# Kernel tuning notes

Measured on AMD Instinct MI355X. Metric: run time of the kernel, lower is better.

The kernel has to match this reference:

```python
import jax, jax.numpy as jnp
import numpy as np

NINP = 1024
NHID = 1024
STEPS = 8
INITRANGE = 0.04
T, B = 256, 64

# DARTS_V1 recurrent genotype: (activation, predecessor-state index)
GENOTYPE = [("sigmoid", 0), ("relu", 1), ("relu", 1), ("identity", 1),
            ("tanh", 2), ("sigmoid", 5), ("tanh", 3), ("relu", 5)]

ACT = {
    "tanh": jnp.tanh,
    "relu": jax.nn.relu,
    "sigmoid": jax.nn.sigmoid,
    "identity": lambda x: x,
    "selu": jax.nn.selu,
}


def setup_inputs() -> dict:
    key = jax.random.key(0)
    k_in, k_w0, k_ws = jax.random.split(key, 3)
    inputs = jax.random.normal(k_in, (T, B, NINP), dtype=jnp.float32)
    hidden = jnp.zeros((1, B, NHID), dtype=jnp.float32)
    W0 = jax.random.uniform(k_w0, (NINP + NHID, 2 * NHID),
                            minval=-INITRANGE, maxval=INITRANGE, dtype=jnp.float32)
    Ws = jax.random.uniform(k_ws, (STEPS, NHID, 2 * NHID),
                            minval=-INITRANGE, maxval=INITRANGE, dtype=jnp.float32)
    return {"inputs": inputs, "hidden": hidden, "W0": W0, "Ws": Ws}


def _cell(x, h_prev, W0, Ws):
    # init state: highway combine of gated candidate with previous hidden
    xh = jnp.concatenate([x, h_prev], axis=-1)            # [B, ninp+nhid]
    c0, h0 = jnp.split(xh @ W0, 2, axis=-1)               # [B, nhid] each
    s0 = h_prev + jax.nn.sigmoid(c0) * (jnp.tanh(h0) - h_prev)
    states = [s0]
    for i, (name, pred) in enumerate(GENOTYPE):
        s_prev = states[pred]
        c, h = jnp.split(s_prev @ Ws[i], 2, axis=-1)      # [B, nhid] each
        s = s_prev + jax.nn.sigmoid(c) * (ACT[name](h) - s_prev)
        states.append(s)
    # output = mean over the DAG intermediate states (concat = range(1, steps+1))
    return jnp.mean(jnp.stack(states[1:], axis=0), axis=0)


def reference(inputs, hidden, W0, Ws):
    h0 = hidden[0]                                        # [B, nhid]

    def step(h, x_t):
        h_new = _cell(x_t, h, W0, Ws)
        return h_new, h_new

    _, hiddens = jax.lax.scan(step, h0, inputs)           # [T, B, nhid]
    return hiddens
```

## Files before the change

kernel.cpp:

```cpp
#include <hip/hip_runtime.h>
#include <math.h>


typedef __attribute__((ext_vector_type(8))) _Float16 half8;
typedef __attribute__((ext_vector_type(4))) float f32x4;
typedef __attribute__((ext_vector_type(4))) unsigned int u32x4;
typedef __attribute__((ext_vector_type(8))) unsigned short us8;

#define NH 1024
#define SCALE 2048.f
#define INVS  (1.f/2048.f)
#define WF_BYTES 83886080ull
#define FA_BYTES 1572864ull
#define T_STEPS  256

__device__ __forceinline__ float sigf(float x){ return 1.f/(1.f+__expf(-x)); }
__device__ __forceinline__ void limbs2(float x, _Float16& a, _Float16& b){
    a = (_Float16)x; b = (_Float16)((x - (float)a)*SCALE);
}

struct Pre { const float* W0; const float* Ws; unsigned short* wf; };

__global__ __launch_bounds__(256) void preconv(Pre d) {
    int gid  = blockIdx.x * 4 + (threadIdx.x >> 6);
    int lane = threadIdx.x & 63;
    const float* W; unsigned short* dst; int nks, cg, ks;
    if (gid < 8192) {
        W = d.W0; dst = d.wf; nks = 64; cg = gid >> 6; ks = gid & 63;
    } else {
        int g = gid - 8192; int mm = g >> 12; int wi = g & 4095;
        W   = d.Ws + (size_t)mm * (1024 * 2048);
        dst = d.wf + 8388608ull + (size_t)mm * 4194304ull;
        nks = 32; cg = wi >> 5; ks = wi & 31;
    }
    int c  = cg * 16 + (lane & 15);
    int kb = ks * 32 + (lane >> 4) * 8;
    half8 h0, h1;
    #pragma unroll
    for (int j = 0; j < 8; ++j) {
        _Float16 p, q; limbs2(W[(size_t)(kb + j) * 2048 + c], p, q);
        h0[j] = p; h1[j] = q;
    }
    unsigned short* o = dst + ((size_t)cg * nks + ks) * 1024 + lane * 8;
    *(half8*)o         = h0;
    *(half8*)(o + 512) = h1;
}

__global__ __launch_bounds__(256) void initk(const float* hidden, char* fa, unsigned* flags) {
    int gid = blockIdx.x * 256 + threadIdx.x;
    if (gid < 1536) flags[gid] = (gid < 256) ? 1u : 0u;
    #pragma unroll
    for (int e = 0; e < 4; ++e) {
        int i = gid * 4 + e;
        int row = i >> 10, col = i & 1023;
        int rt = row >> 4, rowf = row & 15;
        int ksp = col >> 5, kin = col & 31;
        int lanep = (kin >> 3) * 16 + rowf;
        size_t off = (size_t)rt * 65536 + ((size_t)ksp * 64 + lanep) * 32 + (kin & 7) * 4;
        _Float16 u0, u1; limbs2(hidden[i], u0, u1);
        unsigned pk = (unsigned)__builtin_bit_cast(unsigned short, u0) |
                      ((unsigned)__builtin_bit_cast(unsigned short, u1) << 16);
        *(unsigned*)(fa + off) = pk;
    }
}

__device__ __forceinline__ void aload(const char* fa, int ks, int lane, half8& a0, half8& a1) {
    const char* p = fa + ((size_t)ks * 64 + lane) * 32;
    us8 q0 = *(const us8*)p;
    us8 q1 = *(const us8*)(p + 16);
    a0 = __builtin_bit_cast(half8, __builtin_shufflevector(q0, q1, 0,2,4,6,8,10,12,14));
    a1 = __builtin_bit_cast(half8, __builtin_shufflevector(q0, q1, 1,3,5,7,9,11,13,15));
}
__device__ __forceinline__ half8 ldw(const unsigned short* p) { return *(const half8*)p; }
__device__ __forceinline__ void mfma6(half8 a0, half8 a1, half8 w0, half8 w1,
                                      f32x4& x0, f32x4& x1) {
    x0 = __builtin_amdgcn_mfma_f32_16x16x32_f16(a0, w0, x0, 0, 0, 0);
    x1 = __builtin_amdgcn_mfma_f32_16x16x32_f16(a0, w1, x1, 0, 0, 0);
    x1 = __builtin_amdgcn_mfma_f32_16x16x32_f16(a1, w0, x1, 0, 0, 0);
}
__device__ __forceinline__ void rwrite1(float* arena, int wave, int lane,
        f32x4 c0, f32x4 c1, f32x4 h0, f32x4 h1) {
    float* b = arena + wave * 512;
    #pragma unroll
    for (int r = 0; r < 4; ++r) {
        b[lane * 4 + r]       = c0[r] + c1[r] * INVS;
        b[256 + lane * 4 + r] = h0[r] + h1[r] * INVS;
    }
}
__device__ __forceinline__ void rsum1(const float* arena, int idx, float& cs, float& hs) {
    float c = 0.f, h = 0.f;
    #pragma unroll
    for (int w = 0; w < 8; ++w) {
        c += arena[w * 512 + idx];
        h += arena[w * 512 + 256 + idx];
    }
    cs = c; hs = h;
}
__device__ __forceinline__ void fstore(char* fa, int offp, float v) {
    _Float16 u0, u1; limbs2(v, u0, u1);
    unsigned pk = (unsigned)__builtin_bit_cast(unsigned short, u0) |
                  ((unsigned)__builtin_bit_cast(unsigned short, u1) << 16);
    __hip_atomic_store((unsigned*)(fa + offp), pk, __ATOMIC_RELAXED, __HIP_MEMORY_SCOPE_AGENT);
}
template<int ACQ>
__device__ __forceinline__ void pollw(unsigned* f, unsigned tgt, int lane) {
    unsigned v = __hip_atomic_load(f + lane, __ATOMIC_RELAXED, __HIP_MEMORY_SCOPE_AGENT);
    while (__ballot(v < tgt)) {
        __builtin_amdgcn_s_sleep(2);
        v = __hip_atomic_load(f + lane, __ATOMIC_RELAXED, __HIP_MEMORY_SCOPE_AGENT);
    }
    if (ACQ)
        (void)__hip_atomic_load(f, __ATOMIC_ACQUIRE, __HIP_MEMORY_SCOPE_AGENT);
}
__device__ __forceinline__ void publish(unsigned* slot, unsigned v) {
    __hip_atomic_store(slot, v, __ATOMIC_RELAXED, __HIP_MEMORY_SCOPE_AGENT);
}

struct PK {
    const float* x; const float* hidden;
    const unsigned short* wf;
    char* fa; unsigned* flags; float* out;
};

__global__ __launch_bounds__(512, 2) void persist(PK p) {
    __shared__ unsigned short slab[65536];
    __shared__ float arena[4096];

    const int tid  = threadIdx.x;
    const int wave = tid >> 6, lane = tid & 63;
    const int l15 = lane & 15, lg = lane >> 4;
    const int lane8 = lane * 8, lg8 = lg * 8;
    const int bx = blockIdx.x;
    const int cg = (bx & 7) * 8 + ((bx >> 3) & 7);
    const int rt = bx >> 6;

    const unsigned short* wf0 = p.wf;
    const unsigned short* wfs[8];
    #pragma unroll
    for (int i = 0; i < 8; ++i) wfs[i] = p.wf + 8388608ull + (size_t)i * 4194304ull;

    char* FAH  = p.fa + (size_t)(0 * 4 + rt) * 65536;
    char* FAS0 = p.fa + (size_t)(1 * 4 + rt) * 65536;
    char* FAS1 = p.fa + (size_t)(2 * 4 + rt) * 65536;
    char* FAS2 = p.fa + (size_t)(3 * 4 + rt) * 65536;
    char* FAS3 = p.fa + (size_t)(4 * 4 + rt) * 65536;
    char* FAS5 = p.fa + (size_t)(5 * 4 + rt) * 65536;
    #define FLG(tn) (p.flags + ((tn) * 4 + rt) * 64)

    #define PFW(dst, wfp) do { \
        _Pragma("unroll") \
        for (int _i = 0; _i < 4; ++_i) { \
            const int _ks = wave * 4 + _i; \
            const unsigned short* _pc = (wfp) + ((size_t)cg * 32 + _ks) * 1024 + lane8; \
            const unsigned short* _ph = (wfp) + ((size_t)(cg + 64) * 32 + _ks) * 1024 + lane8; \
            dst[_i*4+0] = ldw(_pc); dst[_i*4+1] = ldw(_pc + 512); \
            dst[_i*4+2] = ldw(_ph); dst[_i*4+3] = ldw(_ph + 512); } } while (0)
    #define ALD(dst0, dst1, fa) do { \
        _Pragma("unroll") \
        for (int _i = 0; _i < 4; ++_i) aload(fa, wave * 4 + _i, lane, dst0[_i], dst1[_i]); } while (0)
    #define MFM(w, a0v, a1v, X0, X1, Y0, Y1) do { \
        _Pragma("unroll") \
        for (int _i = 0; _i < 4; ++_i) { \
            mfma6(a0v[_i], a1v[_i], w[_i*4+0], w[_i*4+1], X0, X1); \
            mfma6(a0v[_i], a1v[_i], w[_i*4+2], w[_i*4+3], Y0, Y1); } } while (0)

    {
        const u32x4* sc = (const u32x4*)(wf0 + ((size_t)cg * 64 + 32) * 1024);
        const u32x4* sh = (const u32x4*)(wf0 + ((size_t)(cg + 64) * 64 + 32) * 1024);
        u32x4* dst = (u32x4*)slab;
        for (int i = tid; i < 4096; i += 512) { dst[i] = sc[i]; dst[4096 + i] = sh[i]; }
    }

    const int rowf = tid >> 4, colf = tid & 15;
    const size_t opos = (size_t)(rt * 16 + rowf) * NH + cg * 16 + colf;
    const int idx = colf * 4 + (rowf >> 2) * 64 + (rowf & 3);
    int offp;
    {
        int col = cg * 16 + colf;
        int ksp = col >> 5, kin = col & 31;
        int lanep = (kin >> 3) * 16 + rowf;
        offp = (ksp * 64 + lanep) * 32 + (kin & 7) * 4;
    }
    float hprev = 0.f, s0v = 0.f, s1v = 0.f, s2v = 0.f, s3v = 0.f, s5v = 0.f, runsum = 0.f;
    if (tid < 256) hprev = p.hidden[opos];
    const int xrow = rt * 16 + l15;
    __syncthreads();

    for (int t = 0; t < T_STEPS; ++t) {
        const float* xt = p.x + (size_t)t * 65536;

        f32x4 c0 = {}, c1 = {}, h0 = {}, h1 = {};
        {
            half8 xw[16], xa0[4], xa1[4];
            #pragma unroll
            for (int i = 0; i < 4; ++i) {
                const int ks = wave * 4 + i;
                const unsigned short* pc = wf0 + ((size_t)cg * 64 + ks) * 1024 + lane8;
                const unsigned short* ph = wf0 + ((size_t)(cg + 64) * 64 + ks) * 1024 + lane8;
                xw[i*4+0] = ldw(pc); xw[i*4+1] = ldw(pc + 512);
                xw[i*4+2] = ldw(ph); xw[i*4+3] = ldw(ph + 512);
                const float* xp = xt + (size_t)xrow * NH + ks * 32 + lg8;
                float4 v0 = *(const float4*)xp, v1 = *(const float4*)(xp + 4);
                float fv[8] = {v0.x, v0.y, v0.z, v0.w, v1.x, v1.y, v1.z, v1.w};
                #pragma unroll
                for (int j = 0; j < 8; ++j) { _Float16 u, w2; limbs2(fv[j], u, w2); xa0[i][j] = u; xa1[i][j] = w2; }
            }
            if (wave == 7) pollw<1>(FLG(0), t + 1, lane);
            MFM(xw, xa0, xa1, c0, c1, h0, h1);
        }
        __syncthreads();
        {
            half8 ha0[4], ha1[4];
            ALD(ha0, ha1, FAH);
            #pragma unroll
            for (int i = 0; i < 4; ++i) {
                const int kc = wave * 4 + i;
                const unsigned short* pc = &slab[kc * 1024 + lane8];
                const unsigned short* ph = &slab[(kc + 32) * 1024 + lane8];
                mfma6(ha0[i], ha1[i], *(const half8*)pc, *(const half8*)(pc + 512), c0, c1);
                mfma6(ha0[i], ha1[i], *(const half8*)ph, *(const half8*)(ph + 512), h0, h1);
            }
            rwrite1(arena, wave, lane, c0, c1, h0, h1);
        }
        __syncthreads();
        if (tid < 256) {
            float cs, hs; rsum1(arena, idx, cs, hs);
            s0v = hprev + sigf(cs) * (tanhf(hs) - hprev);
            fstore(FAS0, offp, s0v);
        }
        __syncthreads();
        if (tid == 0) publish(FLG(1) + cg, t + 1);

        {
            half8 w0[16];
            PFW(w0, wfs[0]);
            if (wave == 7) pollw<0>(FLG(1), t + 1, lane);
            __syncthreads();
            half8 a0[4], a1[4];
            ALD(a0, a1, FAS0);
            f32x4 X0 = {}, X1 = {}, Y0 = {}, Y1 = {};
            MFM(w0, a0, a1, X0, X1, Y0, Y1);
            rwrite1(arena, wave, lane, X0, X1, Y0, Y1);
        }
        __syncthreads();
        if (tid < 256) {
            float cs, hs; rsum1(arena, idx, cs, hs);
            s1v = s0v + sigf(cs) * (sigf(hs) - s0v);
            fstore(FAS1, offp, s1v);
            runsum = s1v;
        }
        __syncthreads();
        if (tid == 0) publish(FLG(2) + cg, t + 1);

        {
            half8 w1[16], w2[16];
            PFW(w1, wfs[1]);
            PFW(w2, wfs[2]);
            if (wave == 7) pollw<0>(FLG(2), t + 1, lane);
            __syncthreads();
            half8 a0[4], a1[4];
            ALD(a0, a1, FAS1);
            f32x4 X0 = {}, X1 = {}, Y0 = {}, Y1 = {};
            MFM(w1, a0, a1, X0, X1, Y0, Y1);
            half8 w3[16];
            PFW(w3, wfs[3]);
            rwrite1(arena, wave, lane, X0, X1, Y0, Y1);
            __syncthreads();
            if (tid < 256) {
                float cs, hs; rsum1(arena, idx, cs, hs);
                s2v = s1v + sigf(cs) * (fmaxf(hs, 0.f) - s1v);
                fstore(FAS2, offp, s2v);
            }
            __syncthreads();
            if (tid == 0) publish(FLG(3) + cg, t + 1);
            X0 = (f32x4){}; X1 = (f32x4){}; Y0 = (f32x4){}; Y1 = (f32x4){};
            MFM(w2, a0, a1, X0, X1, Y0, Y1);
            rwrite1(arena, wave, lane, X0, X1, Y0, Y1);
            __syncthreads();
            if (tid < 256) {
                float cs, hs; rsum1(arena, idx, cs, hs);
                s3v = s1v + sigf(cs) * (fmaxf(hs, 0.f) - s1v);
                fstore(FAS3, offp, s3v);
            }
            __syncthreads();
            if (tid == 0) publish(FLG(4) + cg, t + 1);
            X0 = (f32x4){}; X1 = (f32x4){}; Y0 = (f32x4){}; Y1 = (f32x4){};
            MFM(w3, a0, a1, X0, X1, Y0, Y1);
            rwrite1(arena, wave, lane, X0, X1, Y0, Y1);
            __syncthreads();
            if (tid < 256) {
                float cs, hs; rsum1(arena, idx, cs, hs);
                float s4v = s1v + sigf(cs) * (hs - s1v);
                runsum += s2v + s3v + s4v;
            }
            __syncthreads();
        }

        {
            half8 w4[16], w6[16];
            PFW(w4, wfs[4]);
            PFW(w6, wfs[6]);
            if (wave == 7) { pollw<0>(FLG(3), t + 1, lane); pollw<0>(FLG(4), t + 1, lane); }
            __syncthreads();
            half8 a0[4], a1[4], b0[4], b1[4];
            ALD(a0, a1, FAS2);
            ALD(b0, b1, FAS3);
            f32x4 X0 = {}, X1 = {}, Y0 = {}, Y1 = {};
            MFM(w4, a0, a1, X0, X1, Y0, Y1);
            f32x4 U0 = {}, U1 = {}, V0 = {}, V1 = {};
            MFM(w6, b0, b1, U0, U1, V0, V1);
            rwrite1(arena, wave, lane, X0, X1, Y0, Y1);
            __syncthreads();
            if (tid < 256) {
                float cs, hs; rsum1(arena, idx, cs, hs);
                s5v = s2v + sigf(cs) * (tanhf(hs) - s2v);
                fstore(FAS5, offp, s5v);
            }
            __syncthreads();
            if (tid == 0) publish(FLG(5) + cg, t + 1);
            rwrite1(arena, wave, lane, U0, U1, V0, V1);
            __syncthreads();
            if (tid < 256) {
                float cs, hs; rsum1(arena, idx, cs, hs);
                float s7v = s3v + sigf(cs) * (tanhf(hs) - s3v);
                runsum += s5v + s7v;
            }
            __syncthreads();
        }

        {
            half8 w5[16], w7[16];
            PFW(w5, wfs[5]);
            PFW(w7, wfs[7]);
            if (wave == 7) pollw<0>(FLG(5), t + 1, lane);
            __syncthreads();
            half8 a0[4], a1[4];
            ALD(a0, a1, FAS5);
            f32x4 X0 = {}, X1 = {}, Y0 = {}, Y1 = {};
            MFM(w5, a0, a1, X0, X1, Y0, Y1);
            f32x4 U0 = {}, U1 = {}, V0 = {}, V1 = {};
            MFM(w7, a0, a1, U0, U1, V0, V1);
            rwrite1(arena, wave, lane, X0, X1, Y0, Y1);
            __syncthreads();
            float c6 = 0.f, h6 = 0.f;
            if (tid < 256) rsum1(arena, idx, c6, h6);
            __syncthreads();
            rwrite1(arena, wave, lane, U0, U1, V0, V1);
            __syncthreads();
            if (tid < 256) {
                float c8, h8; rsum1(arena, idx, c8, h8);
                float s6 = s5v + sigf(c6) * (sigf(h6) - s5v);
                float s8 = s5v + sigf(c8) * (fmaxf(h8, 0.f) - s5v);
                float v = 0.125f * (runsum + s6 + s8);
                p.out[(size_t)t * 65536 + opos] = v;
                fstore(FAH, offp, v);
                hprev = v;
            }
            __syncthreads();
            if (tid == 0) publish(FLG(0) + cg, t + 2);
        }
    }
    #undef FLG
    #undef PFW
    #undef ALD
    #undef MFM
}

extern "C" void kernel_launch(void* const* d_in, const int* in_sizes, int n_in,
                              void* d_out, int out_size, void* d_ws, size_t ws_size,
                              hipStream_t stream) {
    (void)in_sizes; (void)n_in; (void)out_size; (void)ws_size;
    const float* inputs = (const float*)d_in[0];
    const float* hidden = (const float*)d_in[1];
    const float* W0     = (const float*)d_in[2];
    const float* Ws     = (const float*)d_in[3];
    float* out = (float*)d_out;

    char* base = (char*)d_ws;
    unsigned short* wf = (unsigned short*)base;
    char* fa = base + WF_BYTES;
    unsigned* flags = (unsigned*)(fa + FA_BYTES);

    initk<<<64, 256, 0, stream>>>(hidden, fa, flags);
    preconv<<<10240, 256, 0, stream>>>(Pre{W0, Ws, wf});

    PK pk{inputs, hidden, wf, fa, flags, out};
    void* args[] = {&pk};
    if (hipLaunchCooperativeKernel((void*)persist, dim3(256), dim3(512), args, 0, stream) != hipSuccess)
        persist<<<256, 512, 0, stream>>>(pk);
}
```

Baseline: 9.706 ms.

## Double-buffer weight fragments in registers across cell steps and use raw barriers

Restructures the per-timestep cell so weight fragments for the next matmul are prefetched into one of two register buffers (wA/wB) while the current one is consumed. Loads now start right after each publish, so global weight-load latency can overlap the reductions and polling. Many __syncthreads are replaced with bare s_barrier or lgkmcnt-wait barriers to cut waitcnt overhead. The cost is higher register pressure, and barriers that no longer wait on vector memory could be unsafe wherever global loads must complete before the barrier.

Result: no change. 9.756 ms (+0.5%).

```diff
diff --git a/kernel.cpp b/kernel.cpp
--- a/kernel.cpp
+++ b/kernel.cpp
@@ -13,6 +13,9 @@
 #define WF_BYTES 83886080ull
 #define FA_BYTES 1572864ull
 #define T_STEPS  256
+
+#define WBAR() asm volatile("s_barrier" ::: "memory")
+#define LBAR() asm volatile("s_waitcnt lgkmcnt(0)\n\ts_barrier" ::: "memory")
 
 __device__ __forceinline__ float sigf(float x){ return 1.f/(1.f+__expf(-x)); }
 __device__ __forceinline__ void limbs2(float x, _Float16& a, _Float16& b){
@@ -155,6 +158,14 @@
             const unsigned short* _ph = (wfp) + ((size_t)(cg + 64) * 32 + _ks) * 1024 + lane8; \
             dst[_i*4+0] = ldw(_pc); dst[_i*4+1] = ldw(_pc + 512); \
             dst[_i*4+2] = ldw(_ph); dst[_i*4+3] = ldw(_ph + 512); } } while (0)
+    #define PFWX(dst) do { \
+        _Pragma("unroll") \
+        for (int _i = 0; _i < 4; ++_i) { \
+            const int _ks = wave * 4 + _i; \
+            const unsigned short* _pc = wf0 + ((size_t)cg * 64 + _ks) * 1024 + lane8; \
+            const unsigned short* _ph = wf0 + ((size_t)(cg + 64) * 64 + _ks) * 1024 + lane8; \
+            dst[_i*4+0] = ldw(_pc); dst[_i*4+1] = ldw(_pc + 512); \
+            dst[_i*4+2] = ldw(_ph); dst[_i*4+3] = ldw(_ph + 512); } } while (0)
     #define ALD(dst0, dst1, fa) do { \
         _Pragma("unroll") \
         for (int _i = 0; _i < 4; ++_i) aload(fa, wave * 4 + _i, lane, dst0[_i], dst1[_i]); } while (0)
@@ -186,29 +197,32 @@
     const int xrow = rt * 16 + l15;
     __syncthreads();
 
+    half8 wA[16], wB[16];
+    PFW(wA, wfs[0]);
+    PFWX(wB);
+
     for (int t = 0; t < T_STEPS; ++t) {
         const float* xt = p.x + (size_t)t * 65536;
 
         f32x4 c0 = {}, c1 = {}, h0 = {}, h1 = {};
         {
-            half8 xw[16], xa0[4], xa1[4];
+            half8 xa0[4], xa1[4];
             #pragma unroll
             for (int i = 0; i < 4; ++i) {
                 const int ks = wave * 4 + i;
-                const unsigned short* pc = wf0 + ((size_t)cg * 64 + ks) * 1024 + lane8;
-                const unsigned short* ph = wf0 + ((size_t)(cg + 64) * 64 + ks) * 1024 + lane8;
-                xw[i*4+0] = ldw(pc); xw[i*4+1] = ldw(pc + 512);
-                xw[i*4+2] = ldw(ph); xw[i*4+3] = ldw(ph + 512);
                 const float* xp = xt + (size_t)xrow * NH + ks * 32 + lg8;
                 float4 v0 = *(const float4*)xp, v1 = *(const float4*)(xp + 4);
                 float fv[8] = {v0.x, v0.y, v0.z, v0.w, v1.x, v1.y, v1.z, v1.w};
                 #pragma unroll
                 for (int j = 0; j < 8; ++j) { _Float16 u, w2; limbs2(fv[j], u, w2); xa0[i][j] = u; xa1[i][j] = w2; }
             }
-            if (wave == 7) pollw<1>(FLG(0), t + 1, lane);
-            MFM(xw, xa0, xa1, c0, c1, h0, h1);
-        }
-        __syncthreads();
+            if (wave == 7) {
+                pollw<1>(FLG(0), t + 1, lane);
+                asm volatile("s_waitcnt vmcnt(0)" ::: "memory");
+            }
+            MFM(wB, xa0, xa1, c0, c1, h0, h1);
+        }
+        WBAR();
         {
             half8 ha0[4], ha1[4];
             ALD(ha0, ha1, FAH);
@@ -222,7 +236,7 @@
             }
             rwrite1(arena, wave, lane, c0, c1, h0, h1);
         }
-        __syncthreads();
+        LBAR();
         if (tid < 256) {
             float cs, hs; rsum1(arena, idx, cs, hs);
             s0v = hprev + sigf(cs) * (tanhf(hs) - hprev);
@@ -230,19 +244,18 @@
         }
         __syncthreads();
         if (tid == 0) publish(FLG(1) + cg, t + 1);
-
-        {
-            half8 w0[16];
-            PFW(w0, wfs[0]);
-            if (wave == 7) pollw<0>(FLG(1), t + 1, lane);
-            __syncthreads();
-            half8 a0[4], a1[4];
+        PFW(wB, wfs[1]);
+
+        if (wave == 7) pollw<0>(FLG(1), t + 1, lane);
+        WBAR();
+        half8 a0[4], a1[4];
+        {
             ALD(a0, a1, FAS0);
             f32x4 X0 = {}, X1 = {}, Y0 = {}, Y1 = {};
-            MFM(w0, a0, a1, X0, X1, Y0, Y1);
-            rwrite1(arena, wave, lane, X0, X1, Y0, Y1);
-        }
-        __syncthreads();
+            MFM(wA, a0, a1, X0, X1, Y0, Y1);
+            rwrite1(arena, wave, lane, X0, X1, Y0, Y1);
+        }
+        LBAR();
         if (tid < 256) {
             float cs, hs; rsum1(arena, idx, cs, hs);
             s1v = s0v + sigf(cs) * (sigf(hs) - s0v);
@@ -251,66 +264,65 @@
         }
         __syncthreads();
         if (tid == 0) publish(FLG(2) + cg, t + 1);
-
-        {
-            half8 w1[16], w2[16];
-            PFW(w1, wfs[1]);
-            PFW(w2, wfs[2]);
-            if (wave == 7) pollw<0>(FLG(2), t + 1, lane);
-            __syncthreads();
-            half8 a0[4], a1[4];
-            ALD(a0, a1, FAS1);
-            f32x4 X0 = {}, X1 = {}, Y0 = {}, Y1 = {};
-            MFM(w1, a0, a1, X0, X1, Y0, Y1);
-            half8 w3[16];
-            PFW(w3, wfs[3]);
-            rwrite1(arena, wave, lane, X0, X1, Y0, Y1);
-            __syncthreads();
-            if (tid < 256) {
-                float cs, hs; rsum1(arena, idx, cs, hs);
-                s2v = s1v + sigf(cs) * (fmaxf(hs, 0.f) - s1v);
-                fstore(FAS2, offp, s2v);
-            }
-            __syncthreads();
-            if (tid == 0) publish(FLG(3) + cg, t + 1);
-            X0 = (f32x4){}; X1 = (f32x4){}; Y0 = (f32x4){}; Y1 = (f32x4){};
-            MFM(w2, a0, a1, X0, X1, Y0, Y1);
-            rwrite1(arena, wave, lane, X0, X1, Y0, Y1);
-            __syncthreads();
-            if (tid < 256) {
-                float cs, hs; rsum1(arena, idx, cs, hs);
-                s3v = s1v + sigf(cs) * (fmaxf(hs, 0.f) - s1v);
-                fstore(FAS3, offp, s3v);
-            }
-            __syncthreads();
-            if (tid == 0) publish(FLG(4) + cg, t + 1);
-            X0 = (f32x4){}; X1 = (f32x4){}; Y0 = (f32x4){}; Y1 = (f32x4){};
-            MFM(w3, a0, a1, X0, X1, Y0, Y1);
-            rwrite1(arena, wave, lane, X0, X1, Y0, Y1);
-            __syncthreads();
-            if (tid < 256) {
-                float cs, hs; rsum1(arena, idx, cs, hs);
-                float s4v = s1v + sigf(cs) * (hs - s1v);
-                runsum += s2v + s3v + s4v;
-            }
-            __syncthreads();
-        }
-
-        {
-            half8 w4[16], w6[16];
-            PFW(w4, wfs[4]);
-            PFW(w6, wfs[6]);
-            if (wave == 7) { pollw<0>(FLG(3), t + 1, lane); pollw<0>(FLG(4), t + 1, lane); }
-            __syncthreads();
-            half8 a0[4], a1[4], b0[4], b1[4];
+        PFW(wA, wfs[2]);
+
+        if (wave == 7) pollw<0>(FLG(2), t + 1, lane);
+        WBAR();
+        ALD(a0, a1, FAS1);
+        {
+            f32x4 X0 = {}, X1 = {}, Y0 = {}, Y1 = {};
+            MFM(wB, a0, a1, X0, X1, Y0, Y1);
+            rwrite1(arena, wave, lane, X0, X1, Y0, Y1);
+        }
+        LBAR();
+        if (tid < 256) {
+            float cs, hs; rsum1(arena, idx, cs, hs);
+            s2v = s1v + sigf(cs) * (fmaxf(hs, 0.f) - s1v);
+            fstore(FAS2, offp, s2v);
+        }
+        __syncthreads();
+        if (tid == 0) publish(FLG(3) + cg, t + 1);
+        PFW(wB, wfs[3]);
+        {
+            f32x4 X0 = {}, X1 = {}, Y0 = {}, Y1 = {};
+            MFM(wA, a0, a1, X0, X1, Y0, Y1);
+            rwrite1(arena, wave, lane, X0, X1, Y0, Y1);
+        }
+        LBAR();
+        if (tid < 256) {
+            float cs, hs; rsum1(arena, idx, cs, hs);
+            s3v = s1v + sigf(cs) * (fmaxf(hs, 0.f) - s1v);
+            fstore(FAS3, offp, s3v);
+        }
+        __syncthreads();
+        if (tid == 0) publish(FLG(4) + cg, t + 1);
+        PFW(wA, wfs[4]);
+        {
+            f32x4 X0 = {}, X1 = {}, Y0 = {}, Y1 = {};
+            MFM(wB, a0, a1, X0, X1, Y0, Y1);
+            rwrite1(arena, wave, lane, X0, X1, Y0, Y1);
+        }
+        LBAR();
+        if (tid < 256) {
+            float cs, hs; rsum1(arena, idx, cs, hs);
+            float s4v = s1v + sigf(cs) * (hs - s1v);
+            runsum += s2v + s3v + s4v;
+        }
+        WBAR();
+        PFW(wB, wfs[6]);
+
+        if (wave == 7) { pollw<0>(FLG(3), t + 1, lane); pollw<0>(FLG(4), t + 1, lane); }
+        WBAR();
+        {
+            half8 b0[4], b1[4];
             ALD(a0, a1, FAS2);
             ALD(b0, b1, FAS3);
             f32x4 X0 = {}, X1 = {}, Y0 = {}, Y1 = {};
-            MFM(w4, a0, a1, X0, X1, Y0, Y1);
+            MFM(wA, a0, a1, X0, X1, Y0, Y1);
             f32x4 U0 = {}, U1 = {}, V0 = {}, V1 = {};
-            MFM(w6, b0, b1, U0, U1, V0, V1);
-            rwrite1(arena, wave, lane, X0, X1, Y0, Y1);
-            __syncthreads();
+            MFM(wB, b0, b1, U0, U1, V0, V1);
+            rwrite1(arena, wave, lane, X0, X1, Y0, Y1);
+            LBAR();
             if (tid < 256) {
                 float cs, hs; rsum1(arena, idx, cs, hs);
                 s5v = s2v + sigf(cs) * (tanhf(hs) - s2v);
@@ -318,35 +330,34 @@
             }
             __syncthreads();
             if (tid == 0) publish(FLG(5) + cg, t + 1);
+            PFW(wA, wfs[5]);
             rwrite1(arena, wave, lane, U0, U1, V0, V1);
-            __syncthreads();
+            LBAR();
             if (tid < 256) {
                 float cs, hs; rsum1(arena, idx, cs, hs);
                 float s7v = s3v + sigf(cs) * (tanhf(hs) - s3v);
                 runsum += s5v + s7v;
             }
-            __syncthreads();
-        }
-
-        {
-            half8 w5[16], w7[16];
-            PFW(w5, wfs[5]);
-            PFW(w7, wfs[7]);
-            if (wave == 7) pollw<0>(FLG(5), t + 1, lane);
-            __syncthreads();
-            half8 a0[4], a1[4];
+            WBAR();
+            PFW(wB, wfs[7]);
+        }
+
+        if (wave == 7) pollw<0>(FLG(5), t + 1, lane);
+        WBAR();
+        {
             ALD(a0, a1, FAS5);
             f32x4 X0 = {}, X1 = {}, Y0 = {}, Y1 = {};
-            MFM(w5, a0, a1, X0, X1, Y0, Y1);
+            MFM(wA, a0, a1, X0, X1, Y0, Y1);
             f32x4 U0 = {}, U1 = {}, V0 = {}, V1 = {};
-            MFM(w7, a0, a1, U0, U1, V0, V1);
-            rwrite1(arena, wave, lane, X0, X1, Y0, Y1);
-            __syncthreads();
+            MFM(wB, a0, a1, U0, U1, V0, V1);
+            rwrite1(arena, wave, lane, X0, X1, Y0, Y1);
+            LBAR();
             float c6 = 0.f, h6 = 0.f;
             if (tid < 256) rsum1(arena, idx, c6, h6);
-            __syncthreads();
+            LBAR();
+            PFW(wA, wfs[0]);
             rwrite1(arena, wave, lane, U0, U1, V0, V1);
-            __syncthreads();
+            LBAR();
             if (tid < 256) {
                 float c8, h8; rsum1(arena, idx, c8, h8);
                 float s6 = s5v + sigf(c6) * (sigf(h6) - s5v);
@@ -358,10 +369,12 @@
             }
             __syncthreads();
             if (tid == 0) publish(FLG(0) + cg, t + 2);
+            PFWX(wB);
         }
     }
     #undef FLG
     #undef PFW
+    #undef PFWX
     #undef ALD
     #undef MFM
 }
```

## Use LDS-only barriers and single-wave vectorized reductions in the recurrent cell

Applied to the files above, without the earlier changes.

Replaces most __syncthreads calls with a raw s_barrier that waits only on the LDS counter (lgkmcnt), so outstanding global weight prefetches no longer stall each reduction barrier. The per-step partial-sum reduction now uses float4 LDS writes and reads, done by one wave handling four rows per thread instead of 256 scalar threads. It also adds an extra weight prefetch into a dying register array, apparently to warm the cache for the next stage. The risk is that the custom barrier drops memory-fence semantics, and putting the epilogue on a single wave lengthens its serial transcendental work.

After: 12.65 ms. 1.3x slower.

```diff
diff --git a/kernel.cpp b/kernel.cpp
--- a/kernel.cpp
+++ b/kernel.cpp
@@ -13,6 +13,8 @@
 #define WF_BYTES 83886080ull
 #define FA_BYTES 1572864ull
 #define T_STEPS  256
+
+#define LBAR() asm volatile("s_waitcnt lgkmcnt(0)\n\ts_barrier" ::: "memory")
 
 __device__ __forceinline__ float sigf(float x){ return 1.f/(1.f+__expf(-x)); }
 __device__ __forceinline__ void limbs2(float x, _Float16& a, _Float16& b){
@@ -81,18 +83,18 @@
 __device__ __forceinline__ void rwrite1(float* arena, int wave, int lane,
         f32x4 c0, f32x4 c1, f32x4 h0, f32x4 h1) {
     float* b = arena + wave * 512;
+    f32x4 cv, hv;
     #pragma unroll
-    for (int r = 0; r < 4; ++r) {
-        b[lane * 4 + r]       = c0[r] + c1[r] * INVS;
-        b[256 + lane * 4 + r] = h0[r] + h1[r] * INVS;
-    }
-}
-__device__ __forceinline__ void rsum1(const float* arena, int idx, float& cs, float& hs) {
-    float c = 0.f, h = 0.f;
+    for (int r = 0; r < 4; ++r) { cv[r] = c0[r] + c1[r] * INVS; hv[r] = h0[r] + h1[r] * INVS; }
+    *(f32x4*)(b + lane * 4)       = cv;
+    *(f32x4*)(b + 256 + lane * 4) = hv;
+}
+__device__ __forceinline__ void rsumq(const float* arena, int e, f32x4& cs, f32x4& hs) {
+    f32x4 c = {}, h = {};
     #pragma unroll
     for (int w = 0; w < 8; ++w) {
-        c += arena[w * 512 + idx];
-        h += arena[w * 512 + 256 + idx];
+        c += *(const f32x4*)(arena + w * 512 + e * 4);
+        h += *(const f32x4*)(arena + w * 512 + 256 + e * 4);
     }
     cs = c; hs = h;
 }
@@ -171,18 +173,21 @@
         for (int i = tid; i < 4096; i += 512) { dst[i] = sc[i]; dst[4096 + i] = sh[i]; }
     }
 
-    const int rowf = tid >> 4, colf = tid & 15;
-    const size_t opos = (size_t)(rt * 16 + rowf) * NH + cg * 16 + colf;
-    const int idx = colf * 4 + (rowf >> 2) * 64 + (rowf & 3);
-    int offp;
-    {
-        int col = cg * 16 + colf;
-        int ksp = col >> 5, kin = col & 31;
-        int lanep = (kin >> 3) * 16 + rowf;
-        offp = (ksp * 64 + lanep) * 32 + (kin & 7) * 4;
-    }
-    float hprev = 0.f, s0v = 0.f, s1v = 0.f, s2v = 0.f, s3v = 0.f, s5v = 0.f, runsum = 0.f;
-    if (tid < 256) hprev = p.hidden[opos];
+    size_t opos[4] = {0, 0, 0, 0};
+    int offp[4] = {0, 0, 0, 0};
+    float hprev[4] = {}, s0v[4] = {}, s1v[4] = {}, s2v[4] = {}, s3v[4] = {}, s5v[4] = {}, runsum[4] = {};
+    if (tid < 64) {
+        const int colf = tid & 15, rq = (tid >> 4) * 4;
+        const int col = cg * 16 + colf;
+        const int ksp = col >> 5, kin = col & 31;
+        #pragma unroll
+        for (int r = 0; r < 4; ++r) {
+            const int rowf = rq + r;
+            opos[r] = (size_t)(rt * 16 + rowf) * NH + col;
+            offp[r] = (ksp * 64 + (kin >> 3) * 16 + rowf) * 32 + (kin & 7) * 4;
+            hprev[r] = p.hidden[opos[r]];
+        }
+    }
     const int xrow = rt * 16 + l15;
     __syncthreads();
 
@@ -222,11 +227,14 @@
             }
             rwrite1(arena, wave, lane, c0, c1, h0, h1);
         }
-        __syncthreads();
-        if (tid < 256) {
-            float cs, hs; rsum1(arena, idx, cs, hs);
-            s0v = hprev + sigf(cs) * (tanhf(hs) - hprev);
-            fstore(FAS0, offp, s0v);
+        LBAR();
+        if (tid < 64) {
+            f32x4 cs, hs; rsumq(arena, tid, cs, hs);
+            #pragma unroll
+            for (int r = 0; r < 4; ++r) {
+                s0v[r] = hprev[r] + sigf(cs[r]) * (tanhf(hs[r]) - hprev[r]);
+                fstore(FAS0, offp[r], s0v[r]);
+            }
         }
         __syncthreads();
         if (tid == 0) publish(FLG(1) + cg, t + 1);
@@ -242,12 +250,15 @@
             MFM(w0, a0, a1, X0, X1, Y0, Y1);
             rwrite1(arena, wave, lane, X0, X1, Y0, Y1);
         }
-        __syncthreads();
-        if (tid < 256) {
-            float cs, hs; rsum1(arena, idx, cs, hs);
-            s1v = s0v + sigf(cs) * (sigf(hs) - s0v);
-            fstore(FAS1, offp, s1v);
-            runsum = s1v;
+        LBAR();
+        if (tid < 64) {
+            f32x4 cs, hs; rsumq(arena, tid, cs, hs);
+            #pragma unroll
+            for (int r = 0; r < 4; ++r) {
+                s1v[r] = s0v[r] + sigf(cs[r]) * (sigf(hs[r]) - s0v[r]);
+                fstore(FAS1, offp[r], s1v[r]);
+                runsum[r] = s1v[r];
+            }
         }
         __syncthreads();
         if (tid == 0) publish(FLG(2) + cg, t + 1);
@@ -265,33 +276,42 @@
             half8 w3[16];
             PFW(w3, wfs[3]);
             rwrite1(arena, wave, lane, X0, X1, Y0, Y1);
-            __syncthreads();
-            if (tid < 256) {
-                float cs, hs; rsum1(arena, idx, cs, hs);
-                s2v = s1v + sigf(cs) * (fmaxf(hs, 0.f) - s1v);
-                fstore(FAS2, offp, s2v);
+            LBAR();
+            if (tid < 64) {
+                f32x4 cs, hs; rsumq(arena, tid, cs, hs);
+                #pragma unroll
+                for (int r = 0; r < 4; ++r) {
+                    s2v[r] = s1v[r] + sigf(cs[r]) * (fmaxf(hs[r], 0.f) - s1v[r]);
+                    fstore(FAS2, offp[r], s2v[r]);
+                }
             }
             __syncthreads();
             if (tid == 0) publish(FLG(3) + cg, t + 1);
             X0 = (f32x4){}; X1 = (f32x4){}; Y0 = (f32x4){}; Y1 = (f32x4){};
             MFM(w2, a0, a1, X0, X1, Y0, Y1);
             rwrite1(arena, wave, lane, X0, X1, Y0, Y1);
-            __syncthreads();
-            if (tid < 256) {
-                float cs, hs; rsum1(arena, idx, cs, hs);
-                s3v = s1v + sigf(cs) * (fmaxf(hs, 0.f) - s1v);
-                fstore(FAS3, offp, s3v);
+            LBAR();
+            if (tid < 64) {
+                f32x4 cs, hs; rsumq(arena, tid, cs, hs);
+                #pragma unroll
+                for (int r = 0; r < 4; ++r) {
+                    s3v[r] = s1v[r] + sigf(cs[r]) * (fmaxf(hs[r], 0.f) - s1v[r]);
+                    fstore(FAS3, offp[r], s3v[r]);
+                }
             }
             __syncthreads();
             if (tid == 0) publish(FLG(4) + cg, t + 1);
             X0 = (f32x4){}; X1 = (f32x4){}; Y0 = (f32x4){}; Y1 = (f32x4){};
             MFM(w3, a0, a1, X0, X1, Y0, Y1);
             rwrite1(arena, wave, lane, X0, X1, Y0, Y1);
-            __syncthreads();
-            if (tid < 256) {
-                float cs, hs; rsum1(arena, idx, cs, hs);
-                float s4v = s1v + sigf(cs) * (hs - s1v);
-                runsum += s2v + s3v + s4v;
+            LBAR();
+            if (tid < 64) {
+                f32x4 cs, hs; rsumq(arena, tid, cs, hs);
+                #pragma unroll
+                for (int r = 0; r < 4; ++r) {
+                    float s4 = s1v[r] + sigf(cs[r]) * (hs[r] - s1v[r]);
+                    runsum[r] += s2v[r] + s3v[r] + s4;
+                }
             }
             __syncthreads();
         }
@@ -310,22 +330,29 @@
             f32x4 U0 = {}, U1 = {}, V0 = {}, V1 = {};
             MFM(w6, b0, b1, U0, U1, V0, V1);
             rwrite1(arena, wave, lane, X0, X1, Y0, Y1);
-            __syncthreads();
-            if (tid < 256) {
-                float cs, hs; rsum1(arena, idx, cs, hs);
-                s5v = s2v + sigf(cs) * (tanhf(hs) - s2v);
-                fstore(FAS5, offp, s5v);
+            LBAR();
+            if (tid < 64) {
+                f32x4 cs, hs; rsumq(arena, tid, cs, hs);
+                #pragma unroll
+                for (int r = 0; r < 4; ++r) {
+                    s5v[r] = s2v[r] + sigf(cs[r]) * (tanhf(hs[r]) - s2v[r]);
+                    fstore(FAS5, offp[r], s5v[r]);
+                }
             }
             __syncthreads();
             if (tid == 0) publish(FLG(5) + cg, t + 1);
             rwrite1(arena, wave, lane, U0, U1, V0, V1);
-            __syncthreads();
-            if (tid < 256) {
-                float cs, hs; rsum1(arena, idx, cs, hs);
-                float s7v = s3v + sigf(cs) * (tanhf(hs) - s3v);
-                runsum += s5v + s7v;
-            }
-            __syncthreads();
+            LBAR();
+            if (tid < 64) {
+                f32x4 cs, hs; rsumq(arena, tid, cs, hs);
+                #pragma unroll
+                for (int r = 0; r < 4; ++r) {
+                    float s7 = s3v[r] + sigf(cs[r]) * (tanhf(hs[r]) - s3v[r]);
+                    runsum[r] += s5v[r] + s7;
+                }
+            }
+            __syncthreads();
+            PFW(w4, wfs[5]);
         }
 
         {
@@ -341,20 +368,23 @@
             f32x4 U0 = {}, U1 = {}, V0 = {}, V1 = {};
             MFM(w7, a0, a1, U0, U1, V0, V1);
             rwrite1(arena, wave, lane, X0, X1, Y0, Y1);
-            __syncthreads();
-            float c6 = 0.f, h6 = 0.f;
-            if (tid < 256) rsum1(arena, idx, c6, h6);
-            __syncthreads();
+            LBAR();
+            f32x4 c6 = {}, h6 = {};
+            if (tid < 64) rsumq(arena, tid, c6, h6);
+            LBAR();
             rwrite1(arena, wave, lane, U0, U1, V0, V1);
-            __syncthreads();
-            if (tid < 256) {
-                float c8, h8; rsum1(arena, idx, c8, h8);
-                float s6 = s5v + sigf(c6) * (sigf(h6) - s5v);
-                float s8 = s5v + sigf(c8) * (fmaxf(h8, 0.f) - s5v);
-                float v = 0.125f * (runsum + s6 + s8);
-                p.out[(size_t)t * 65536 + opos] = v;
-                fstore(FAH, offp, v);
-                hprev = v;
+            LBAR();
+            if (tid < 64) {
+                f32x4 c8, h8; rsumq(arena, tid, c8, h8);
+                #pragma unroll
+                for (int r = 0; r < 4; ++r) {
+                    float s6 = s5v[r] + sigf(c6[r]) * (sigf(h6[r]) - s5v[r]);
+                    float s8 = s5v[r] + sigf(c8[r]) * (fmaxf(h8[r], 0.f) - s5v[r]);
+                    float v = 0.125f * (runsum[r] + s6 + s8);
+                    p.out[(size_t)t * 65536 + opos[r]] = v;
+                    fstore(FAH, offp[r], v);
+                    hprev[r] = v;
+                }
             }
             __syncthreads();
             if (tid == 0) publish(FLG(0) + cg, t + 2);
```

## Precompute input projection x@W0 in a separate kernel before the recurrent loop

Applied to the files above, without the earlier changes.

Adds a pre-pass kernel that computes the input half of the first-layer GEMM for all timesteps and stores the c/h pre-activations in workspace. When the workspace is large enough, the persistent recurrent kernel reads these values instead of doing the x-part MFMAs each step, which shortens the serial critical path. It also swaps several __syncthreads for a barrier that only waits on LDS counters. The cost is an extra 128MB workspace buffer plus a separate kernel pass, and the fast path only runs if ws_size is large enough.

Measured after the change: 9.554 ms. No clear change (-1.6%).

```diff
diff --git a/kernel.cpp b/kernel.cpp
--- a/kernel.cpp
+++ b/kernel.cpp
@@ -12,7 +12,10 @@
 #define INVS  (1.f/2048.f)
 #define WF_BYTES 83886080ull
 #define FA_BYTES 1572864ull
+#define XW_BYTES 134217728ull
 #define T_STEPS  256
+
+#define LBAR() asm volatile("s_waitcnt lgkmcnt(0)\n\ts_barrier" ::: "memory")
 
 __device__ __forceinline__ float sigf(float x){ return 1.f/(1.f+__expf(-x)); }
 __device__ __forceinline__ void limbs2(float x, _Float16& a, _Float16& b){
@@ -116,12 +119,64 @@
     __hip_atomic_store(slot, v, __ATOMIC_RELAXED, __HIP_MEMORY_SCOPE_AGENT);
 }
 
+struct XPK { const float* x; const unsigned short* wf; float* xw; };
+
+__global__ __launch_bounds__(512, 2) void xw0_gemm(XPK p) {
+    __shared__ float arena[4096];
+    const int tid  = threadIdx.x;
+    const int wave = tid >> 6, lane = tid & 63;
+    const int l15 = lane & 15, lg = lane >> 4;
+    const int lane8 = lane * 8, lg8 = lg * 8;
+    const int bx = blockIdx.x;
+    const int cg = (bx & 7) * 8 + ((bx >> 3) & 7);
+    const int rt = bx >> 6;
+    const unsigned short* wf0 = p.wf;
+    const int xrow = rt * 16 + l15;
+    const int rowf = tid >> 4, colf = tid & 15;
+    const size_t opos = (size_t)(rt * 16 + rowf) * NH + cg * 16 + colf;
+    const int idx = colf * 4 + (rowf >> 2) * 64 + (rowf & 3);
+
+    for (int t = 0; t < T_STEPS; ++t) {
+        const float* xt = p.x + (size_t)t * 65536;
+        f32x4 c0 = {}, c1 = {}, h0 = {}, h1 = {};
+        half8 xw_[16], xa0[4], xa1[4];
+        #pragma unroll
+        for (int i = 0; i < 4; ++i) {
+            const int ks = wave * 4 + i;
+            const unsigned short* pc = wf0 + ((size_t)cg * 64 + ks) * 1024 + lane8;
+            const unsigned short* ph = wf0 + ((size_t)(cg + 64) * 64 + ks) * 1024 + lane8;
+            xw_[i*4+0] = ldw(pc); xw_[i*4+1] = ldw(pc + 512);
+            xw_[i*4+2] = ldw(ph); xw_[i*4+3] = ldw(ph + 512);
+            const float* xp = xt + (size_t)xrow * NH + ks * 32 + lg8;
+            float4 v0 = *(const float4*)xp, v1 = *(const float4*)(xp + 4);
+            float fv[8] = {v0.x, v0.y, v0.z, v0.w, v1.x, v1.y, v1.z, v1.w};
+            #pragma unroll
+            for (int j = 0; j < 8; ++j) { _Float16 u, w2; limbs2(fv[j], u, w2); xa0[i][j] = u; xa1[i][j] = w2; }
+        }
+        #pragma unroll
+        for (int i = 0; i < 4; ++i) {
+            mfma6(xa0[i], xa1[i], xw_[i*4+0], xw_[i*4+1], c0, c1);
+            mfma6(xa0[i], xa1[i], xw_[i*4+2], xw_[i*4+3], h0, h1);
+        }
+        rwrite1(arena, wave, lane, c0, c1, h0, h1);
+        LBAR();
+        if (tid < 256) {
+            float cs, hs; rsum1(arena, idx, cs, hs);
+            p.xw[(size_t)t * 131072 + opos]         = cs;
+            p.xw[(size_t)t * 131072 + 65536 + opos] = hs;
+        }
+        __syncthreads();
+    }
+}
+
 struct PK {
     const float* x; const float* hidden;
     const unsigned short* wf;
     char* fa; unsigned* flags; float* out;
+    const float* xw;
 };
 
+template<int XPRE>
 __global__ __launch_bounds__(512, 2) void persist(PK p) {
     __shared__ unsigned short slab[65536];
     __shared__ float arena[4096];
@@ -190,15 +245,22 @@
         const float* xt = p.x + (size_t)t * 65536;
 
         f32x4 c0 = {}, c1 = {}, h0 = {}, h1 = {};
-        {
-            half8 xw[16], xa0[4], xa1[4];
+        float xcv = 0.f, xhv = 0.f;
+        if constexpr (XPRE) {
+            if (tid < 256) {
+                xcv = p.xw[(size_t)t * 131072 + opos];
+                xhv = p.xw[(size_t)t * 131072 + 65536 + opos];
+            }
+            if (wave == 7) pollw<1>(FLG(0), t + 1, lane);
+        } else {
+            half8 xw_[16], xa0[4], xa1[4];
             #pragma unroll
             for (int i = 0; i < 4; ++i) {
                 const int ks = wave * 4 + i;
                 const unsigned short* pc = wf0 + ((size_t)cg * 64 + ks) * 1024 + lane8;
                 const unsigned short* ph = wf0 + ((size_t)(cg + 64) * 64 + ks) * 1024 + lane8;
-                xw[i*4+0] = ldw(pc); xw[i*4+1] = ldw(pc + 512);
-                xw[i*4+2] = ldw(ph); xw[i*4+3] = ldw(ph + 512);
+                xw_[i*4+0] = ldw(pc); xw_[i*4+1] = ldw(pc + 512);
+                xw_[i*4+2] = ldw(ph); xw_[i*4+3] = ldw(ph + 512);
                 const float* xp = xt + (size_t)xrow * NH + ks * 32 + lg8;
                 float4 v0 = *(const float4*)xp, v1 = *(const float4*)(xp + 4);
                 float fv[8] = {v0.x, v0.y, v0.z, v0.w, v1.x, v1.y, v1.z, v1.w};
@@ -206,7 +268,7 @@
                 for (int j = 0; j < 8; ++j) { _Float16 u, w2; limbs2(fv[j], u, w2); xa0[i][j] = u; xa1[i][j] = w2; }
             }
             if (wave == 7) pollw<1>(FLG(0), t + 1, lane);
-            MFM(xw, xa0, xa1, c0, c1, h0, h1);
+            MFM(xw_, xa0, xa1, c0, c1, h0, h1);
         }
         __syncthreads();
         {
@@ -222,9 +284,10 @@
             }
             rwrite1(arena, wave, lane, c0, c1, h0, h1);
         }
-        __syncthreads();
+        LBAR();
         if (tid < 256) {
             float cs, hs; rsum1(arena, idx, cs, hs);
+            if constexpr (XPRE) { cs += xcv; hs += xhv; }
             s0v = hprev + sigf(cs) * (tanhf(hs) - hprev);
             fstore(FAS0, offp, s0v);
         }
@@ -242,7 +305,7 @@
             MFM(w0, a0, a1, X0, X1, Y0, Y1);
             rwrite1(arena, wave, lane, X0, X1, Y0, Y1);
         }
-        __syncthreads();
+        LBAR();
         if (tid < 256) {
             float cs, hs; rsum1(arena, idx, cs, hs);
             s1v = s0v + sigf(cs) * (sigf(hs) - s0v);
@@ -276,7 +339,7 @@
             X0 = (f32x4){}; X1 = (f32x4){}; Y0 = (f32x4){}; Y1 = (f32x4){};
             MFM(w2, a0, a1, X0, X1, Y0, Y1);
             rwrite1(arena, wave, lane, X0, X1, Y0, Y1);
-            __syncthreads();
+            LBAR();
             if (tid < 256) {
                 float cs, hs; rsum1(arena, idx, cs, hs);
                 s3v = s1v + sigf(cs) * (fmaxf(hs, 0.f) - s1v);
@@ -287,7 +350,7 @@
             X0 = (f32x4){}; X1 = (f32x4){}; Y0 = (f32x4){}; Y1 = (f32x4){};
             MFM(w3, a0, a1, X0, X1, Y0, Y1);
             rwrite1(arena, wave, lane, X0, X1, Y0, Y1);
-            __syncthreads();
+            LBAR();
             if (tid < 256) {
                 float cs, hs; rsum1(arena, idx, cs, hs);
                 float s4v = s1v + sigf(cs) * (hs - s1v);
@@ -310,7 +373,7 @@
             f32x4 U0 = {}, U1 = {}, V0 = {}, V1 = {};
             MFM(w6, b0, b1, U0, U1, V0, V1);
             rwrite1(arena, wave, lane, X0, X1, Y0, Y1);
-            __syncthreads();
+            LBAR();
             if (tid < 256) {
                 float cs, hs; rsum1(arena, idx, cs, hs);
                 s5v = s2v + sigf(cs) * (tanhf(hs) - s2v);
@@ -319,7 +382,7 @@
             __syncthreads();
             if (tid == 0) publish(FLG(5) + cg, t + 1);
             rwrite1(arena, wave, lane, U0, U1, V0, V1);
-            __syncthreads();
+            LBAR();
             if (tid < 256) {
                 float cs, hs; rsum1(arena, idx, cs, hs);
                 float s7v = s3v + sigf(cs) * (tanhf(hs) - s3v);
@@ -341,12 +404,12 @@
             f32x4 U0 = {}, U1 = {}, V0 = {}, V1 = {};
             MFM(w7, a0, a1, U0, U1, V0, V1);
             rwrite1(arena, wave, lane, X0, X1, Y0, Y1);
-            __syncthreads();
+            LBAR();
             float c6 = 0.f, h6 = 0.f;
             if (tid < 256) rsum1(arena, idx, c6, h6);
-            __syncthreads();
+            LBAR();
             rwrite1(arena, wave, lane, U0, U1, V0, V1);
-            __syncthreads();
+            LBAR();
             if (tid < 256) {
                 float c8, h8; rsum1(arena, idx, c8, h8);
                 float s6 = s5v + sigf(c6) * (sigf(h6) - s5v);
@@ -369,7 +432,7 @@
 extern "C" void kernel_launch(void* const* d_in, const int* in_sizes, int n_in,
                               void* d_out, int out_size, void* d_ws, size_t ws_size,
                               hipStream_t stream) {
-    (void)in_sizes; (void)n_in; (void)out_size; (void)ws_size;
+    (void)in_sizes; (void)n_in; (void)out_size;
     const float* inputs = (const float*)d_in[0];
     const float* hidden = (const float*)d_in[1];
     const float* W0     = (const float*)d_in[2];
@@ -380,12 +443,24 @@
     unsigned short* wf = (unsigned short*)base;
     char* fa = base + WF_BYTES;
     unsigned* flags = (unsigned*)(fa + FA_BYTES);
+    float* xw = (float*)(fa + FA_BYTES + 8192);
+
+    const size_t NEED_XW = WF_BYTES + FA_BYTES + 8192 + XW_BYTES;
+    const bool xpre = ws_size >= NEED_XW;
 
     initk<<<64, 256, 0, stream>>>(hidden, fa, flags);
     preconv<<<10240, 256, 0, stream>>>(Pre{W0, Ws, wf});
-
-    PK pk{inputs, hidden, wf, fa, flags, out};
+    if (xpre) xw0_gemm<<<256, 512, 0, stream>>>(XPK{inputs, wf, xw});
+
+    PK pk{inputs, hidden, wf, fa, flags, out, xpre ? xw : (const float*)0};
     void* args[] = {&pk};
-    if (hipLaunchCooperativeKernel((void*)persist, dim3(256), dim3(512), args, 0, stream) != hipSuccess)
-        persist<<<256, 512, 0, stream>>>(pk);
-}
+    if (xpre) {
+        auto fn = persist<1>;
+        if (hipLaunchCooperativeKernel((void*)fn, dim3(256), dim3(512), args, 0, stream) != hipSuccess)
+            persist<1><<<256, 512, 0, stream>>>(pk);
+    } else {
+        auto fn = persist<0>;
+        if (hipLaunchCooperativeKernel((void*)fn, dim3(256), dim3(512), args, 0, stream) != hipSuccess)
+            persist<0><<<256, 512, 0, stream>>>(pk);
+    }
+}
```
